# Optimization experiments

Hardware: AMD Instinct MI355X
Metric: run time of the kernel (lower is better)

## Reference

```python
import jax, jax.numpy as jnp
import numpy as np

N_NODES = 100000
N_EDGES = 1600000
D_IN = 128
D_OUT = 128
LN_EPS = 1e-5
MEAN_EPS = 1e-8


def setup_inputs() -> dict:
    key = jax.random.key(0)
    ks = jax.random.split(key, 8)
    x = jax.random.normal(ks[0], (N_NODES, D_IN), dtype=jnp.float32)
    edge_index = jax.random.randint(ks[1], (2, N_EDGES), 0, N_NODES, dtype=jnp.int64)
    s = 1.0 / np.sqrt(D_IN)
    W_agg = jax.random.uniform(ks[2], (D_OUT, D_IN), jnp.float32, -s, s)
    b_agg = jax.random.uniform(ks[3], (D_OUT,), jnp.float32, -s, s)
    W_self = jax.random.uniform(ks[4], (D_OUT, D_IN), jnp.float32, -s, s)
    b_self = jax.random.uniform(ks[5], (D_OUT,), jnp.float32, -s, s)
    gamma = jnp.ones((D_OUT,), jnp.float32)
    beta = jnp.zeros((D_OUT,), jnp.float32)
    return {"x": x, "edge_index": edge_index, "W_agg": W_agg, "b_agg": b_agg,
            "W_self": W_self, "b_self": b_self, "gamma": gamma, "beta": beta}


def reference(x, edge_index, W_agg, b_agg, W_self, b_self, gamma, beta):
    row, col = edge_index[0], edge_index[1]
    num_nodes = x.shape[0]
    # self path: Linear(in, out)
    self_out = x @ W_self.T + b_self                              # [N, D_OUT]
    # mean aggregation: fused gather + segment-sum (no index_add buffer passes)
    neighbor_sum = jax.ops.segment_sum(x[col], row, num_segments=num_nodes)   # [N, D_IN]
    ones = jnp.ones((col.shape[0], 1), dtype=x.dtype)
    neighbor_count = jax.ops.segment_sum(ones, row, num_segments=num_nodes)   # [N, 1]
    neighbor_mean = neighbor_sum / (neighbor_count + MEAN_EPS)
    agg_out = neighbor_mean @ W_agg.T + b_agg                     # [N, D_OUT]
    # relu -> LayerNorm (dropout is identity at eval)
    h = jax.nn.relu(self_out + agg_out)
    mu = jnp.mean(h, axis=-1, keepdims=True)
    var = jnp.mean(jnp.square(h - mu), axis=-1, keepdims=True)
    return (h - mu) * jax.lax.rsqrt(var + LN_EPS) * gamma + beta
```

## Files before the change

kernel.cpp:

```cpp
#include <hip/hip_runtime.h>

#define N_NODES 100000
#define N_EDGES 1600000
#define D 128
#define RPB 64
#define NBUCKET 1563
#define NBLK 196
#define EPB 8192
#define AGG_CAP 2048
#define XCB 3125
#define SCAN_PAD 1792

constexpr float LN_EPS   = 1e-5f;
constexpr float MEAN_EPS = 1e-8f;

typedef __attribute__((ext_vector_type(8))) short bf16x8;
typedef __attribute__((ext_vector_type(4))) float f32x4;
typedef __attribute__((ext_vector_type(2))) float f32x2;
typedef __attribute__((ext_vector_type(4))) unsigned uint4e;
typedef __attribute__((ext_vector_type(2))) unsigned uint2e;

__device__ inline unsigned short f2bf(float f) {
  union { float f; unsigned u; } v; v.f = f;
  return (unsigned short)((v.u + 0x7FFFu + ((v.u >> 16) & 1u)) >> 16);
}
__device__ inline unsigned pack2(float a, float b) {
  return (unsigned)f2bf(a) | ((unsigned)f2bf(b) << 16);
}

__global__ __launch_bounds__(256) void prep_sort(
    const float* __restrict__ x, const int* __restrict__ ei,
    const float* __restrict__ Wself, const float* __restrict__ Wagg,
    const float* __restrict__ bself, const float* __restrict__ bagg,
    unsigned short* __restrict__ xb, unsigned char* __restrict__ x8,
    unsigned short* __restrict__ wcat, float* __restrict__ bsum,
    unsigned* __restrict__ ent_sorted, int* __restrict__ chunkoff) {
  __shared__ int ent_s[EPB];
  __shared__ int cnt_s[SCAN_PAD];
  __shared__ int off_s[SCAN_PAD];
  __shared__ int sb[256];
  const int bid = blockIdx.x;
  const int t = threadIdx.x;

  if (bid < NBLK) {
    const int ebase = bid * EPB;
    const int nch = min(EPB, N_EDGES - ebase);
    const int base4 = bid * (EPB / 4);
    const int end4 = base4 + (nch >> 2);

    for (int i = t; i < SCAN_PAD; i += 256) cnt_s[i] = 0;
    __syncthreads();

#pragma unroll
    for (int k = 0; k < EPB / 1024; ++k) {
      int i4 = base4 + k * 256 + t;
      if (i4 < end4) {
        int4 r = ((const int4*)ei)[i4];
        atomicAdd(&cnt_s[r.x >> 6], 1);
        atomicAdd(&cnt_s[r.y >> 6], 1);
        atomicAdd(&cnt_s[r.z >> 6], 1);
        atomicAdd(&cnt_s[r.w >> 6], 1);
      }
    }
    __syncthreads();

    int psum = 0;
#pragma unroll
    for (int i = 0; i < 7; ++i) psum += cnt_s[t * 7 + i];
    sb[t] = psum;
    __syncthreads();
    for (int off = 1; off < 256; off <<= 1) {
      int u = (t >= off) ? sb[t - off] : 0;
      __syncthreads();
      sb[t] += u;
      __syncthreads();
    }
    int run = sb[t] - psum;
#pragma unroll
    for (int i = 0; i < 7; ++i) {
      off_s[t * 7 + i] = run;
      run += cnt_s[t * 7 + i];
    }
    __syncthreads();

    for (int b = t; b < NBUCKET; b += 256)
      chunkoff[b * NBLK + bid] = off_s[b] | (cnt_s[b] << 14);
    __syncthreads();

#pragma unroll
    for (int k = 0; k < EPB / 1024; ++k) {
      int i4 = base4 + k * 256 + t;
      if (i4 < end4) {
        int4 r = ((const int4*)ei)[i4];
        int4 c = ((const int4*)(ei + N_EDGES))[i4];
        int p0 = atomicAdd(&off_s[r.x >> 6], 1);
        ent_s[p0] = ((r.x & 63) << 17) | c.x;
        int p1 = atomicAdd(&off_s[r.y >> 6], 1);
        ent_s[p1] = ((r.y & 63) << 17) | c.y;
        int p2 = atomicAdd(&off_s[r.z >> 6], 1);
        ent_s[p2] = ((r.z & 63) << 17) | c.z;
        int p3 = atomicAdd(&off_s[r.w >> 6], 1);
        ent_s[p3] = ((r.w & 63) << 17) | c.w;
      }
    }
    __syncthreads();

    for (int i = t; i < nch; i += 256)
      ent_sorted[ebase + i] = (unsigned)ent_s[i];
  } else if (bid < NBLK + XCB) {
    const int f = (bid - NBLK) * 4096 + t * 16;
    const float4 v0 = ((const float4*)x)[(f >> 2) + 0];
    const float4 v1 = ((const float4*)x)[(f >> 2) + 1];
    const float4 v2 = ((const float4*)x)[(f >> 2) + 2];
    const float4 v3 = ((const float4*)x)[(f >> 2) + 3];
    uint4e lo, hi;
    lo.x = pack2(v0.x, v0.y); lo.y = pack2(v0.z, v0.w);
    lo.z = pack2(v1.x, v1.y); lo.w = pack2(v1.z, v1.w);
    hi.x = pack2(v2.x, v2.y); hi.y = pack2(v2.z, v2.w);
    hi.z = pack2(v3.x, v3.y); hi.w = pack2(v3.z, v3.w);
    *(uint4e*)(xb + f) = lo;
    *(uint4e*)(xb + f + 8) = hi;
    unsigned q0 = 0, q1 = 0, q2 = 0, q3 = 0;
    q0 = __builtin_amdgcn_cvt_pk_fp8_f32(v0.x, v0.y, q0, false);
    q0 = __builtin_amdgcn_cvt_pk_fp8_f32(v0.z, v0.w, q0, true);
    q1 = __builtin_amdgcn_cvt_pk_fp8_f32(v1.x, v1.y, q1, false);
    q1 = __builtin_amdgcn_cvt_pk_fp8_f32(v1.z, v1.w, q1, true);
    q2 = __builtin_amdgcn_cvt_pk_fp8_f32(v2.x, v2.y, q2, false);
    q2 = __builtin_amdgcn_cvt_pk_fp8_f32(v2.z, v2.w, q2, true);
    q3 = __builtin_amdgcn_cvt_pk_fp8_f32(v3.x, v3.y, q3, false);
    q3 = __builtin_amdgcn_cvt_pk_fp8_f32(v3.z, v3.w, q3, true);
    uint4e q; q.x = q0; q.y = q1; q.z = q2; q.w = q3;
    *(uint4e*)(x8 + f) = q;
  } else {
    const int blk = bid - NBLK - XCB;
#pragma unroll
    for (int k = 0; k < 8; ++k) {
      int idx = blk * 2048 + k * 256 + t;
      int o = idx >> 8, kc = idx & 255;
      float v = (kc < 128) ? Wself[o * 128 + kc] : Wagg[o * 128 + (kc - 128)];
      wcat[o * 256 + kc] = f2bf(v);
    }
    if (blk == 0 && t < 128) bsum[t] = bself[t] + bagg[t];
    if (blk == 0 && t < 32)
      *(unsigned*)(x8 + (size_t)N_NODES * 128 + t * 4) = 0u;
  }
}

__global__ __launch_bounds__(256) void aggregate(
    const unsigned char* __restrict__ x8, const unsigned* __restrict__ ent_sorted,
    const int* __restrict__ chunkoff, float* out) {
  __shared__ int ent_s[AGG_CAP];
  __shared__ int col_s[AGG_CAP + 16];
  __shared__ int sb[256];
  __shared__ int cnt_s[RPB];
  __shared__ int off_s[RPB];
  __shared__ int cur_s[RPB];

  const int b = blockIdx.x;
  const int t = threadIdx.x;

  int beg = 0, len = 0;
  if (t < NBLK) {
    int pk = chunkoff[b * NBLK + t];
    beg = pk & 16383;
    len = pk >> 14;
  }
  sb[t] = len;
  __syncthreads();
  for (int off = 1; off < 256; off <<= 1) {
    int u = (t >= off) ? sb[t - off] : 0;
    __syncthreads();
    sb[t] += u;
    __syncthreads();
  }
  int n = sb[255]; if (n > AGG_CAP) n = AGG_CAP;
  int dst = sb[t] - len;
  if (t < NBLK) {
    const unsigned* src = ent_sorted + t * EPB + beg;
    for (int i = 0; i < len; ++i)
      if (dst + i < AGG_CAP) ent_s[dst + i] = (int)src[i];
  }
  __syncthreads();

  if (t < RPB) cnt_s[t] = 0;
  __syncthreads();
  for (int i = t; i < n; i += 256) atomicAdd(&cnt_s[ent_s[i] >> 17], 1);
  __syncthreads();
  if (t < RPB) off_s[t] = cnt_s[t];
  __syncthreads();
  for (int off = 1; off < RPB; off <<= 1) {
    int u = 0;
    if (t < RPB && t >= off) u = off_s[t - off];
    __syncthreads();
    if (t < RPB) off_s[t] += u;
    __syncthreads();
  }
  int excl = 0;
  if (t < RPB) excl = off_s[t] - cnt_s[t];
  __syncthreads();
  if (t < RPB) { off_s[t] = excl; cur_s[t] = excl; }
  __syncthreads();
  for (int i = t; i < n; i += 256) {
    int e = ent_s[i];
    int pos = atomicAdd(&cur_s[e >> 17], 1);
    col_s[pos] = e & 0x1FFFF;
  }
  __syncthreads();

  const int w = t >> 6, lane = t & 63;
  const int half = lane >> 5, lq = lane & 31;
  const int nodebase = b << 6;
  for (int lrow = w; lrow < RPB; lrow += 4) {
    int node = nodebase + lrow;
    if (node >= N_NODES) break;
    int rbeg = off_s[lrow];
    int deg = cnt_s[lrow];
    float a0 = 0.f, a1 = 0.f, a2 = 0.f, a3 = 0.f;
    for (int j0 = 0; j0 < deg; j0 += 16) {
      unsigned p[8];
#pragma unroll
      for (int u = 0; u < 8; ++u) {
        int idx = j0 + u * 2 + half;
        int col = col_s[rbeg + idx];
        col = (idx < deg) ? col : N_NODES;
        p[u] = *(const unsigned*)(x8 + (size_t)col * 128 + lq * 4);
      }
#pragma unroll
      for (int u = 0; u < 8; ++u) {
        f32x2 lo = __builtin_amdgcn_cvt_pk_f32_fp8(p[u], false);
        f32x2 hi = __builtin_amdgcn_cvt_pk_f32_fp8(p[u], true);
        a0 += lo.x; a1 += lo.y; a2 += hi.x; a3 += hi.y;
      }
    }
    a0 += __shfl_xor(a0, 32, 64);
    a1 += __shfl_xor(a1, 32, 64);
    a2 += __shfl_xor(a2, 32, 64);
    a3 += __shfl_xor(a3, 32, 64);
    if (half == 0) {
      float inv = 1.0f / ((float)deg + MEAN_EPS);
      uint2e o;
      o.x = pack2(a0 * inv, a1 * inv);
      o.y = pack2(a2 * inv, a3 * inv);
      *(uint2e*)((unsigned short*)(out + (size_t)node * D) + lq * 4) = o;
    }
  }
}

__global__ __launch_bounds__(512, 4) void gemm_mfma_ln(
    const unsigned short* __restrict__ xb, const float* out_mean,
    const unsigned short* __restrict__ wcat, const float* __restrict__ bsum,
    const float* __restrict__ gamma, const float* __restrict__ beta,
    float* out) {
  __shared__ unsigned short Bs[128 * 264];
  __shared__ float bias_s[128];

  const int t = threadIdx.x;
  const int w = t >> 6, lane = t & 63;
  const int q = lane >> 4, s = lane & 15;
  const int base = blockIdx.x * 128;

  if (t < 128) bias_s[t] = bsum[t];

#pragma unroll
  for (int r = 0; r < 8; ++r) {
    int f = r * 512 + t;
    int row = f >> 5, c = f & 31;
    uint4 v = *(const uint4*)(wcat + row * 256 + c * 8);
    *(uint4*)(Bs + row * 264 + c * 8) = v;
  }

  const int arow = base + w * 16 + s;
  const int asafe = (arow < N_NODES) ? arow : 0;
  const unsigned short* xrow = xb + (size_t)asafe * 128;
  const unsigned short* mrow = (const unsigned short*)(out_mean + (size_t)asafe * 128);
  bf16x8 a[8];
#pragma unroll
  for (int kk = 0; kk < 4; ++kk)
    a[kk] = *(const bf16x8*)(xrow + kk * 32 + q * 8);
#pragma unroll
  for (int kk = 0; kk < 4; ++kk)
    a[4 + kk] = *(const bf16x8*)(mrow + kk * 32 + q * 8);

  __syncthreads();

  f32x4 acc[8];
#pragma unroll
  for (int j = 0; j < 8; ++j) acc[j] = (f32x4)(0.0f);

#pragma unroll
  for (int kk = 0; kk < 8; ++kk) {
    const int ko = kk * 32 + q * 8;
#pragma unroll
    for (int j = 0; j < 8; ++j) {
      bf16x8 bv = *(const bf16x8*)(Bs + (j * 16 + s) * 264 + ko);
      acc[j] = __builtin_amdgcn_mfma_f32_16x16x32_bf16(a[kk], bv, acc[j], 0, 0, 0);
    }
  }

#pragma unroll
  for (int j = 0; j < 8; ++j) {
    float bb = bias_s[j * 16 + s];
#pragma unroll
    for (int r = 0; r < 4; ++r)
      acc[j][r] = fmaxf(acc[j][r] + bb, 0.0f);
  }

  float g[8], be[8];
#pragma unroll
  for (int j = 0; j < 8; ++j) {
    g[j]  = gamma[j * 16 + s];
    be[j] = beta[j * 16 + s];
  }

#pragma unroll
  for (int r = 0; r < 4; ++r) {
    float s1 = 0.f, s2 = 0.f;
#pragma unroll
    for (int j = 0; j < 8; ++j) {
      float h = acc[j][r];
      s1 += h; s2 += h * h;
    }
#pragma unroll
    for (int m = 1; m < 16; m <<= 1) {
      s1 += __shfl_xor(s1, m, 64);
      s2 += __shfl_xor(s2, m, 64);
    }
    int node = base + w * 16 + q * 4 + r;
    if (node < N_NODES) {
      float mu = s1 * (1.0f / 128.0f);
      float var = s2 * (1.0f / 128.0f) - mu * mu;
      float rstd = rsqrtf(var + LN_EPS);
      float* orow = out + (size_t)node * 128;
#pragma unroll
      for (int j = 0; j < 8; ++j)
        orow[j * 16 + s] = (acc[j][r] - mu) * rstd * g[j] + be[j];
    }
  }
}

extern "C" void kernel_launch(void* const* d_in, const int* in_sizes, int n_in,
                              void* d_out, int out_size, void* d_ws, size_t ws_size,
                              hipStream_t stream) {
  const float* x     = (const float*)d_in[0];
  const int*   ei    = (const int*)d_in[1];
  const float* Wagg  = (const float*)d_in[2];
  const float* bagg  = (const float*)d_in[3];
  const float* Wself = (const float*)d_in[4];
  const float* bself = (const float*)d_in[5];
  const float* gamma = (const float*)d_in[6];
  const float* beta  = (const float*)d_in[7];
  float* out = (float*)d_out;

  unsigned short* xb   = (unsigned short*)d_ws;
  unsigned char*  x8   = (unsigned char*)(xb + (size_t)N_NODES * D);
  unsigned short* wcat = (unsigned short*)(x8 + (size_t)(N_NODES + 1) * D);
  float* bsum      = (float*)(wcat + 128 * 256);
  unsigned* ent_sorted = (unsigned*)(bsum + 128);
  int* chunkoff    = (int*)(ent_sorted + (size_t)NBLK * EPB);

  prep_sort<<<NBLK + XCB + 16, 256, 0, stream>>>(
      x, ei, Wself, Wagg, bself, bagg, xb, x8, wcat, bsum, ent_sorted, chunkoff);

  aggregate<<<NBUCKET, 256, 0, stream>>>(x8, ent_sorted, chunkoff, out);

  gemm_mfma_ln<<<(N_NODES + 127) / 128, 512, 0, stream>>>(
      xb, out, wcat, bsum, gamma, beta, out);
}
```

Measured before the change: 205.9 us.

## Use wave shuffle scans and gather two rows per wave in aggregate

```diff
diff --git a/kernel.cpp b/kernel.cpp
--- a/kernel.cpp
+++ b/kernel.cpp
@@ -150,14 +150,15 @@
     const unsigned char* __restrict__ x8, const unsigned* __restrict__ ent_sorted,
     const int* __restrict__ chunkoff, float* out) {
   __shared__ int ent_s[AGG_CAP];
-  __shared__ int col_s[AGG_CAP + 16];
-  __shared__ int sb[256];
+  __shared__ int col_s[AGG_CAP];
   __shared__ int cnt_s[RPB];
   __shared__ int off_s[RPB];
   __shared__ int cur_s[RPB];
+  __shared__ int wsum[4];
 
   const int b = blockIdx.x;
   const int t = threadIdx.x;
+  const int w = t >> 6, lane = t & 63;
 
   int beg = 0, len = 0;
   if (t < NBLK) {
@@ -165,16 +166,20 @@
     beg = pk & 16383;
     len = pk >> 14;
   }
-  sb[t] = len;
-  __syncthreads();
-  for (int off = 1; off < 256; off <<= 1) {
-    int u = (t >= off) ? sb[t - off] : 0;
-    __syncthreads();
-    sb[t] += u;
-    __syncthreads();
-  }
-  int n = sb[255]; if (n > AGG_CAP) n = AGG_CAP;
-  int dst = sb[t] - len;
+  int v = len;
+#pragma unroll
+  for (int off = 1; off < 64; off <<= 1) {
+    int u = __shfl_up(v, off, 64);
+    if (lane >= off) v += u;
+  }
+  if (lane == 63) wsum[w] = v;
+  if (t < RPB) cnt_s[t] = 0;
+  __syncthreads();
+  int pre = 0;
+  for (int i = 0; i < w; ++i) pre += wsum[i];
+  int n = wsum[0] + wsum[1] + wsum[2] + wsum[3];
+  if (n > AGG_CAP) n = AGG_CAP;
+  int dst = pre + v - len;
   if (t < NBLK) {
     const unsigned* src = ent_sorted + t * EPB + beg;
     for (int i = 0; i < len; ++i)
@@ -182,24 +187,22 @@
   }
   __syncthreads();
 
-  if (t < RPB) cnt_s[t] = 0;
-  __syncthreads();
   for (int i = t; i < n; i += 256) atomicAdd(&cnt_s[ent_s[i] >> 17], 1);
   __syncthreads();
-  if (t < RPB) off_s[t] = cnt_s[t];
-  __syncthreads();
-  for (int off = 1; off < RPB; off <<= 1) {
-    int u = 0;
-    if (t < RPB && t >= off) u = off_s[t - off];
-    __syncthreads();
-    if (t < RPB) off_s[t] += u;
-    __syncthreads();
-  }
-  int excl = 0;
-  if (t < RPB) excl = off_s[t] - cnt_s[t];
-  __syncthreads();
-  if (t < RPB) { off_s[t] = excl; cur_s[t] = excl; }
-  __syncthreads();
+
+  if (t < RPB) {
+    int c = cnt_s[t];
+    int sv = c;
+#pragma unroll
+    for (int off = 1; off < 64; off <<= 1) {
+      int u = __shfl_up(sv, off, 64);
+      if (t >= off) sv += u;
+    }
+    off_s[t] = sv - c;
+    cur_s[t] = sv - c;
+  }
+  __syncthreads();
+
   for (int i = t; i < n; i += 256) {
     int e = ent_s[i];
     int pos = atomicAdd(&cur_s[e >> 17], 1);
@@ -207,41 +210,65 @@
   }
   __syncthreads();
 
-  const int w = t >> 6, lane = t & 63;
   const int half = lane >> 5, lq = lane & 31;
   const int nodebase = b << 6;
-  for (int lrow = w; lrow < RPB; lrow += 4) {
-    int node = nodebase + lrow;
-    if (node >= N_NODES) break;
-    int rbeg = off_s[lrow];
-    int deg = cnt_s[lrow];
-    float a0 = 0.f, a1 = 0.f, a2 = 0.f, a3 = 0.f;
-    for (int j0 = 0; j0 < deg; j0 += 16) {
-      unsigned p[8];
+  for (int r0 = w; r0 < 32; r0 += 4) {
+    const int rA = r0, rB = r0 + 32;
+    const int begA = off_s[rA], degA = cnt_s[rA];
+    const int begB = off_s[rB], degB = cnt_s[rB];
+    const int dmax = max(degA, degB);
+    float aA0 = 0.f, aA1 = 0.f, aA2 = 0.f, aA3 = 0.f;
+    float aB0 = 0.f, aB1 = 0.f, aB2 = 0.f, aB3 = 0.f;
+    for (int j0 = 0; j0 < dmax; j0 += 16) {
+      unsigned pA[8], pB[8];
 #pragma unroll
       for (int u = 0; u < 8; ++u) {
         int idx = j0 + u * 2 + half;
-        int col = col_s[rbeg + idx];
-        col = (idx < deg) ? col : N_NODES;
-        p[u] = *(const unsigned*)(x8 + (size_t)col * 128 + lq * 4);
+        int cA = col_s[(begA + idx) & (AGG_CAP - 1)];
+        cA = (idx < degA) ? cA : N_NODES;
+        pA[u] = *(const unsigned*)(x8 + (size_t)cA * 128 + lq * 4);
+        int cB = col_s[(begB + idx) & (AGG_CAP - 1)];
+        cB = (idx < degB) ? cB : N_NODES;
+        pB[u] = *(const unsigned*)(x8 + (size_t)cB * 128 + lq * 4);
       }
 #pragma unroll
       for (int u = 0; u < 8; ++u) {
-        f32x2 lo = __builtin_amdgcn_cvt_pk_f32_fp8(p[u], false);
-        f32x2 hi = __builtin_amdgcn_cvt_pk_f32_fp8(p[u], true);
-        a0 += lo.x; a1 += lo.y; a2 += hi.x; a3 += hi.y;
-      }
-    }
-    a0 += __shfl_xor(a0, 32, 64);
-    a1 += __shfl_xor(a1, 32, 64);
-    a2 += __shfl_xor(a2, 32, 64);
-    a3 += __shfl_xor(a3, 32, 64);
+        f32x2 lo = __builtin_amdgcn_cvt_pk_f32_fp8(pA[u], false);
+        f32x2 hi = __builtin_amdgcn_cvt_pk_f32_fp8(pA[u], true);
+        aA0 += lo.x; aA1 += lo.y; aA2 += hi.x; aA3 += hi.y;
+      }
+#pragma unroll
+      for (int u = 0; u < 8; ++u) {
+        f32x2 lo = __builtin_amdgcn_cvt_pk_f32_fp8(pB[u], false);
+        f32x2 hi = __builtin_amdgcn_cvt_pk_f32_fp8(pB[u], true);
+        aB0 += lo.x; aB1 += lo.y; aB2 += hi.x; aB3 += hi.y;
+      }
+    }
+    aA0 += __shfl_xor(aA0, 32, 64);
+    aA1 += __shfl_xor(aA1, 32, 64);
+    aA2 += __shfl_xor(aA2, 32, 64);
+    aA3 += __shfl_xor(aA3, 32, 64);
+    aB0 += __shfl_xor(aB0, 32, 64);
+    aB1 += __shfl_xor(aB1, 32, 64);
+    aB2 += __shfl_xor(aB2, 32, 64);
+    aB3 += __shfl_xor(aB3, 32, 64);
     if (half == 0) {
-      float inv = 1.0f / ((float)deg + MEAN_EPS);
-      uint2e o;
-      o.x = pack2(a0 * inv, a1 * inv);
-      o.y = pack2(a2 * inv, a3 * inv);
-      *(uint2e*)((unsigned short*)(out + (size_t)node * D) + lq * 4) = o;
+      int nodeA = nodebase + rA;
+      if (nodeA < N_NODES) {
+        float inv = 1.0f / ((float)degA + MEAN_EPS);
+        uint2e o;
+        o.x = pack2(aA0 * inv, aA1 * inv);
+        o.y = pack2(aA2 * inv, aA3 * inv);
+        *(uint2e*)((unsigned short*)(out + (size_t)nodeA * D) + lq * 4) = o;
+      }
+      int nodeB = nodebase + rB;
+      if (nodeB < N_NODES) {
+        float inv = 1.0f / ((float)degB + MEAN_EPS);
+        uint2e o;
+        o.x = pack2(aB0 * inv, aB1 * inv);
+        o.y = pack2(aB2 * inv, aB3 * inv);
+        *(uint2e*)((unsigned short*)(out + (size_t)nodeB * D) + lq * 4) = o;
+      }
     }
   }
 }
```

After: 213.3 us. 1.04x slower.

## Split each aggregate bucket across two blocks by half-bucket bit

Applied to the files above, without the earlier changes.

```diff
diff --git a/kernel.cpp b/kernel.cpp
--- a/kernel.cpp
+++ b/kernel.cpp
@@ -7,7 +7,7 @@
 #define NBUCKET 1563
 #define NBLK 196
 #define EPB 8192
-#define AGG_CAP 2048
+#define HCAP 1024
 #define XCB 3125
 #define SCAN_PAD 1792
 
@@ -149,15 +149,18 @@
 __global__ __launch_bounds__(256) void aggregate(
     const unsigned char* __restrict__ x8, const unsigned* __restrict__ ent_sorted,
     const int* __restrict__ chunkoff, float* out) {
-  __shared__ int ent_s[AGG_CAP];
-  __shared__ int col_s[AGG_CAP + 16];
-  __shared__ int sb[256];
-  __shared__ int cnt_s[RPB];
-  __shared__ int off_s[RPB];
-  __shared__ int cur_s[RPB];
-
-  const int b = blockIdx.x;
+  __shared__ int ent_s[HCAP];
+  __shared__ int col_s[HCAP];
+  __shared__ int cnt_s[32];
+  __shared__ int off_s[32];
+  __shared__ int cur_s[32];
+  __shared__ int nh;
+
+  const int bid = blockIdx.x;
+  const int b = bid >> 1;
+  const unsigned hb = (unsigned)(bid & 1);
   const int t = threadIdx.x;
+  const int w = t >> 6, lane = t & 63;
 
   int beg = 0, len = 0;
   if (t < NBLK) {
@@ -165,63 +168,68 @@
     beg = pk & 16383;
     len = pk >> 14;
   }
-  sb[t] = len;
-  __syncthreads();
-  for (int off = 1; off < 256; off <<= 1) {
-    int u = (t >= off) ? sb[t - off] : 0;
-    __syncthreads();
-    sb[t] += u;
-    __syncthreads();
-  }
-  int n = sb[255]; if (n > AGG_CAP) n = AGG_CAP;
-  int dst = sb[t] - len;
-  if (t < NBLK) {
-    const unsigned* src = ent_sorted + t * EPB + beg;
+  if (t == 0) nh = 0;
+  if (t < 32) cnt_s[t] = 0;
+  __syncthreads();
+
+  const unsigned* src = ent_sorted + (size_t)t * EPB + beg;
+  int cnt = 0;
+  if (t < NBLK)
     for (int i = 0; i < len; ++i)
-      if (dst + i < AGG_CAP) ent_s[dst + i] = (int)src[i];
-  }
-  __syncthreads();
-
-  if (t < RPB) cnt_s[t] = 0;
-  __syncthreads();
-  for (int i = t; i < n; i += 256) atomicAdd(&cnt_s[ent_s[i] >> 17], 1);
-  __syncthreads();
-  if (t < RPB) off_s[t] = cnt_s[t];
-  __syncthreads();
-  for (int off = 1; off < RPB; off <<= 1) {
-    int u = 0;
-    if (t < RPB && t >= off) u = off_s[t - off];
-    __syncthreads();
-    if (t < RPB) off_s[t] += u;
-    __syncthreads();
-  }
-  int excl = 0;
-  if (t < RPB) excl = off_s[t] - cnt_s[t];
-  __syncthreads();
-  if (t < RPB) { off_s[t] = excl; cur_s[t] = excl; }
-  __syncthreads();
+      cnt += (int)(((src[i] >> 22) & 1u) == hb);
+  int base = 0;
+  if (cnt) base = atomicAdd(&nh, cnt);
+  __syncthreads();
+  int n = nh; if (n > HCAP) n = HCAP;
+  if (cnt) {
+    int p = base;
+    for (int i = 0; i < len; ++i) {
+      unsigned e = src[i];
+      if (((e >> 22) & 1u) == hb) {
+        if (p < HCAP) ent_s[p] = (int)e;
+        ++p;
+      }
+    }
+  }
+  __syncthreads();
+
+  for (int i = t; i < n; i += 256) atomicAdd(&cnt_s[(ent_s[i] >> 17) & 31], 1);
+  __syncthreads();
+
+  if (t < 32) {
+    int c = cnt_s[t];
+    int sv = c;
+#pragma unroll
+    for (int off = 1; off < 32; off <<= 1) {
+      int u = __shfl_up(sv, off, 64);
+      if (t >= off) sv += u;
+    }
+    off_s[t] = sv - c;
+    cur_s[t] = sv - c;
+  }
+  __syncthreads();
+
   for (int i = t; i < n; i += 256) {
     int e = ent_s[i];
-    int pos = atomicAdd(&cur_s[e >> 17], 1);
-    col_s[pos] = e & 0x1FFFF;
-  }
-  __syncthreads();
-
-  const int w = t >> 6, lane = t & 63;
+    int pos = atomicAdd(&cur_s[(e >> 17) & 31], 1);
+    col_s[pos & (HCAP - 1)] = e & 0x1FFFF;
+  }
+  __syncthreads();
+
   const int half = lane >> 5, lq = lane & 31;
-  const int nodebase = b << 6;
-  for (int lrow = w; lrow < RPB; lrow += 4) {
-    int node = nodebase + lrow;
+  const int nodebase = (b << 6) + ((int)hb << 5);
+  for (int lr = w; lr < 32; lr += 4) {
+    int node = nodebase + lr;
     if (node >= N_NODES) break;
-    int rbeg = off_s[lrow];
-    int deg = cnt_s[lrow];
+    int rbeg = off_s[lr];
+    int deg = cnt_s[lr];
     float a0 = 0.f, a1 = 0.f, a2 = 0.f, a3 = 0.f;
     for (int j0 = 0; j0 < deg; j0 += 16) {
       unsigned p[8];
 #pragma unroll
       for (int u = 0; u < 8; ++u) {
         int idx = j0 + u * 2 + half;
-        int col = col_s[rbeg + idx];
+        int col = col_s[(rbeg + idx) & (HCAP - 1)];
         col = (idx < deg) ? col : N_NODES;
         p[u] = *(const unsigned*)(x8 + (size_t)col * 128 + lq * 4);
       }
@@ -361,7 +369,7 @@
   prep_sort<<<NBLK + XCB + 16, 256, 0, stream>>>(
       x, ei, Wself, Wagg, bself, bagg, xb, x8, wcat, bsum, ent_sorted, chunkoff);
 
-  aggregate<<<NBUCKET, 256, 0, stream>>>(x8, ent_sorted, chunkoff, out);
+  aggregate<<<NBUCKET * 2, 256, 0, stream>>>(x8, ent_sorted, chunkoff, out);
 
   gemm_mfma_ln<<<(N_NODES + 127) / 128, 512, 0, stream>>>(
       xb, out, wcat, bsum, gamma, beta, out);
```

After: 214.0 us. 1.04x slower.
